# Kernel tuning notes

Measured on AMD Instinct MI355X. Metric: run time of the kernel, lower is better.

The kernel has to match this reference:

```python
import jax, jax.numpy as jnp
import numpy as np

B, N, D, E = 4, 1024, 1024, 8
TOP_N = 2
THRESHOLD = 0.2
EPS = 1e-9
CAP_FACTOR = 2.0
MIN_EXPERT_CAPACITY = 4
H = int(D * 4 * 2 / 3)  # GEGLU hidden = 2730


def setup_inputs() -> dict:
    key = jax.random.key(0)
    ks = jax.random.split(key, 8)
    u = lambda k, shape, fan: jax.random.uniform(k, shape, jnp.float32, -1.0, 1.0) * (fan ** -0.5)
    return {
        "x": jax.random.normal(ks[0], (B, N, D), jnp.float32),
        "route_probs": jax.random.uniform(ks[1], (TOP_N, B, N), jnp.float32),
        "gate_w": u(ks[2], (D, E), D),
        "w1": u(ks[3], (E, D, 2 * H), 2 * H),
        "b1": u(ks[4], (E, 2 * H), 2 * H),
        "mult_bias": jnp.ones((E, H), jnp.float32),
        "w2": u(ks[5], (E, H, D), D),
        "b2": u(ks[6], (E, D), D),
    }


def reference(x, route_probs, gate_w, w1, b1, mult_bias, w2, b2):
    b, n, d = x.shape
    e = gate_w.shape[1]
    cap = max(min(n, int(n * CAP_FACTOR / e)), MIN_EXPERT_CAPACITY)  # 256

    # ---- top-n gating ----
    logits = jnp.einsum('bnd,de->bne', x, gate_w)
    raw_gates = jax.nn.softmax(logits, axis=-1)
    gate_vals, gate_idx = jax.lax.top_k(raw_gates, TOP_N)          # [b,n,k]
    gate_vals = jnp.moveaxis(gate_vals, -1, 0)                      # [k,b,n]
    gate_idx = jnp.moveaxis(gate_idx, -1, 0)                        # [k,b,n]
    one_hot_idx = jax.nn.one_hot(gate_idx, e, dtype=x.dtype)        # [k,b,n,e]

    denom = jnp.clip(gate_vals.sum(axis=0, keepdims=True), EPS)
    gate_vals = gate_vals / denom

    # route to expert k>0 with prob min(1, gate/threshold); expert 0 always routed
    should_route = route_probs < (gate_vals / THRESHOLD)
    should_route = should_route.at[0].set(True)
    mask = one_hot_idx * should_route[..., None].astype(x.dtype)    # [k,b,n,e]

    # exclusive cumsum over sequence dim -> position within each expert
    mask_cumsum = jnp.cumsum(mask, axis=2) - mask                   # [k,b,n,e]

    positions, masks = [], []
    prev_count = jnp.zeros((b, 1, e), x.dtype)
    for k in range(TOP_N):  # small fixed loop over top-n
        pos_e = (mask_cumsum[k] + prev_count) * mask[k]             # [b,n,e]
        mk = mask[k] * (pos_e < float(cap)).astype(x.dtype)
        prev_count = prev_count + mk.sum(axis=1, keepdims=True)
        positions.append(pos_e.sum(axis=-1))                        # [b,n]
        masks.append(mk)
    positions = jnp.stack(positions)                                # [k,b,n]
    mask = jnp.stack(masks)                                         # [k,b,n,e]

    mask_flat = mask.sum(axis=-1)                                   # [k,b,n] in {0,1}
    gates = gate_vals * mask_flat
    pos_one_hot = jax.nn.one_hot(positions.astype(jnp.int32), cap, dtype=x.dtype)  # [k,b,n,c]

    # combine tensor [b,n,e,c]; dispatch is its boolean support
    combine = jnp.einsum('kbn,kbne,kbnc->bnec', gates * mask_flat, one_hot_idx, pos_one_hot)
    dispatch = (combine > 0).astype(x.dtype)

    # ---- dispatch tokens to experts ----
    xe = jnp.einsum('bnd,bnec->ebcd', x, dispatch)                  # [e,b,c,d]

    # ---- per-expert GEGLU FFN (grouped GEMM) ----
    h = jnp.einsum('ebcd,edf->ebcf', xe, w1) + b1[:, None, None, :]
    val, gate = jnp.split(h, 2, axis=-1)
    act = jax.nn.gelu(gate, approximate=False) * val * mult_bias[:, None, None, :]
    out_e = jnp.einsum('ebch,ehd->ebcd', act, w2) + b2[:, None, None, :]

    # ---- combine ----
    out = jnp.einsum('ebcd,bnec->bnd', out_e, combine)
    return out


if __name__ == '__main__':
    inp = setup_inputs()
    o = reference(**inp)
    print(o.shape, o.dtype)
```

## Files before the change

kernel.cpp:

```cpp
#include <hip/hip_runtime.h>
#include <hip/hip_bf16.h>
#include <math.h>

#define B_ 4
#define N_ 1024
#define D_ 1024
#define E_ 8
#define H_ 2730
#define H2_ 5460
#define CAP_ 256
#define NTOK 4096
#define NSLOT 8192
#define NKT1 16
#define NK1T 32
#define NKT2 43
#define NK2T 86
#define NFG 22

typedef __attribute__((ext_vector_type(8))) short short8;
typedef __attribute__((ext_vector_type(4))) float f32x4;

__device__ __forceinline__ unsigned short f2bf(float f) {
    __hip_bfloat16 h = __float2bfloat16(f);
    return *reinterpret_cast<unsigned short*>(&h);
}
__device__ __forceinline__ float bf2f(unsigned short u) {
    unsigned x = ((unsigned)u) << 16;
    union { unsigned u; float f; } c; c.u = x; return c.f;
}

#define GLL16(g, l)                                                          \
    __builtin_amdgcn_global_load_lds(                                        \
        (const __attribute__((address_space(1))) void*)(g),                  \
        (__attribute__((address_space(3))) void*)(l), 16, 0, 0)

#define VMCNT0() asm volatile("s_waitcnt vmcnt(0)" ::: "memory")
#define SBAR()   __builtin_amdgcn_s_barrier()
#define SCHEDB() __builtin_amdgcn_sched_barrier(0)
#define MFMA16(a, b, c) __builtin_amdgcn_mfma_f32_16x16x32_bf16((a), (b), (c), 0, 0, 0)


__global__ __launch_bounds__(256) void k_cvt1(const float* __restrict__ w1,
                                              unsigned short* __restrict__ w1p) {
    const int fg = blockIdx.x;
    const int kt = blockIdx.y;
    const int e  = blockIdx.z;
    const float* w1e = w1 + (size_t)e * D_ * H2_;
    unsigned short* dst = w1p + (((size_t)((e * NFG + fg) * NKT1 + kt)) << 14);
#pragma unroll
    for (int i = 0; i < 8; ++i) {
        const int o = i * 256 + threadIdx.x;
        const int l = o & 63, n16 = (o >> 6) & 15, k32 = o >> 10;
        const int f = fg * 128 + ((n16 & 7) << 4) + (l & 15);
        const int k = kt * 64 + (k32 << 5) + ((l >> 4) << 3);
        ushort4 r0 = {0, 0, 0, 0}, r1 = {0, 0, 0, 0};
        if (f < H_) {
            const float* s = w1e + (size_t)k * H2_ + (n16 >= 8 ? H_ : 0) + f;
            r0.x = f2bf(s[0]);
            r0.y = f2bf(s[(size_t)H2_]);
            r0.z = f2bf(s[(size_t)2 * H2_]);
            r0.w = f2bf(s[(size_t)3 * H2_]);
            r1.x = f2bf(s[(size_t)4 * H2_]);
            r1.y = f2bf(s[(size_t)5 * H2_]);
            r1.z = f2bf(s[(size_t)6 * H2_]);
            r1.w = f2bf(s[(size_t)7 * H2_]);
        }
        *reinterpret_cast<ushort4*>(dst + (size_t)o * 8) = r0;
        *reinterpret_cast<ushort4*>(dst + (size_t)o * 8 + 4) = r1;
    }
}

__global__ __launch_bounds__(256) void k_cvt2(const float* __restrict__ w2,
                                              unsigned short* __restrict__ w2p) {
    const int kt = blockIdx.x;
    const int nt = blockIdx.y;
    const int e  = blockIdx.z;
    const float* w2e = w2 + (size_t)e * H_ * D_;
    unsigned short* dst = w2p + (((size_t)((e * 8 + nt) * NKT2 + kt)) << 13);
#pragma unroll
    for (int i = 0; i < 4; ++i) {
        const int o = i * 256 + threadIdx.x;
        const int l = o & 63, n16 = (o >> 6) & 7, k32 = o >> 9;
        const int d = nt * 128 + (n16 << 4) + (l & 15);
        const int f = kt * 64 + (k32 << 5) + ((l >> 4) << 3);
        const float* s = w2e + (size_t)f * D_ + d;
        ushort4 r0, r1;
        r0.x = (f + 0 < H_) ? f2bf(s[0]) : 0;
        r0.y = (f + 1 < H_) ? f2bf(s[(size_t)D_]) : 0;
        r0.z = (f + 2 < H_) ? f2bf(s[(size_t)2 * D_]) : 0;
        r0.w = (f + 3 < H_) ? f2bf(s[(size_t)3 * D_]) : 0;
        r1.x = (f + 4 < H_) ? f2bf(s[(size_t)4 * D_]) : 0;
        r1.y = (f + 5 < H_) ? f2bf(s[(size_t)5 * D_]) : 0;
        r1.z = (f + 6 < H_) ? f2bf(s[(size_t)6 * D_]) : 0;
        r1.w = (f + 7 < H_) ? f2bf(s[(size_t)7 * D_]) : 0;
        *reinterpret_cast<ushort4*>(dst + (size_t)o * 8) = r0;
        *reinterpret_cast<ushort4*>(dst + (size_t)o * 8 + 4) = r1;
    }
}

__global__ __launch_bounds__(256) void k_gate(const float* __restrict__ x,
                                              const float* __restrict__ route,
                                              const float* __restrict__ gw,
                                              int* __restrict__ tokE,
                                              float* __restrict__ tokG,
                                              int* __restrict__ tokR) {
    const int wave = threadIdx.x >> 6, lane = threadIdx.x & 63;
    const int t = blockIdx.x * 4 + wave;
    float acc[E_];
#pragma unroll
    for (int e = 0; e < E_; ++e) acc[e] = 0.f;
    const float* xr = x + (size_t)t * D_;
    for (int d = lane; d < D_; d += 64) {
        float xv = xr[d];
        const float* g = gw + d * E_;
#pragma unroll
        for (int e = 0; e < E_; ++e) acc[e] = fmaf(xv, g[e], acc[e]);
    }
#pragma unroll
    for (int e = 0; e < E_; ++e) {
#pragma unroll
        for (int off = 32; off; off >>= 1) acc[e] += __shfl_xor(acc[e], off);
    }
    if (lane == 0) {
        float m = acc[0];
#pragma unroll
        for (int e = 1; e < E_; ++e) m = fmaxf(m, acc[e]);
        float p[E_]; float s = 0.f;
#pragma unroll
        for (int e = 0; e < E_; ++e) { p[e] = expf(acc[e] - m); s += p[e]; }
        int i0 = 0; float v0 = p[0];
#pragma unroll
        for (int e = 1; e < E_; ++e) if (p[e] > v0) { v0 = p[e]; i0 = e; }
        int i1 = (i0 == 0) ? 1 : 0; float v1 = p[i1];
#pragma unroll
        for (int e = 0; e < E_; ++e) if (e != i0 && p[e] > v1) { v1 = p[e]; i1 = e; }
        float p0 = v0 / s, p1 = v1 / s;
        float denom = fmaxf(p0 + p1, 1e-9f);
        float g0 = p0 / denom, g1 = p1 / denom;
        int r1 = route[NTOK + t] < (g1 / 0.2f);
        tokE[t] = i0; tokE[NTOK + t] = i1;
        tokG[t] = g0; tokG[NTOK + t] = g1;
        tokR[t] = r1;
    }
}

__global__ __launch_bounds__(256) void k_pos(const int* __restrict__ tokE,
                                             const float* __restrict__ tokG,
                                             const int* __restrict__ tokR,
                                             int* __restrict__ sot,
                                             int* __restrict__ tos) {
    const int e = blockIdx.x & 7, b = blockIdx.x >> 3;
    const int t = threadIdx.x;
    __shared__ int sc[256];
    const int base_bt = b * N_ + t * 4;
    int m0[4], m1[4];
    int c0 = 0, c1 = 0;
#pragma unroll
    for (int i = 0; i < 4; ++i) {
        int bt = base_bt + i;
        m0[i] = (tokE[bt] == e) ? 1 : 0;
        m1[i] = ((tokE[NTOK + bt] == e) && tokR[bt]) ? 1 : 0;
        c0 += m0[i]; c1 += m1[i];
    }
    int packed = c0 | (c1 << 16);
    sc[t] = packed;
    __syncthreads();
    for (int off = 1; off < 256; off <<= 1) {
        int v = (t >= off) ? sc[t - off] : 0;
        __syncthreads();
        sc[t] += v;
        __syncthreads();
    }
    int incl = sc[t];
    int total = sc[255];
    int excl = incl - packed;
    int base0 = excl & 0xffff;
    int base1 = excl >> 16;
    int kept0 = min(total & 0xffff, CAP_);
#pragma unroll
    for (int i = 0; i < 4; ++i) {
        int bt = base_bt + i;
        if (m0[i]) {
            int pos = base0++;
            if (pos < CAP_ && tokG[bt] > 0.f) {
                int s = ((e * B_ + b) << 8) + pos;
                sot[bt] = s;
                tos[s] = bt;
            }
        }
        if (m1[i]) {
            int pos = (base1++) + kept0;
            if (pos < CAP_ && tokG[NTOK + bt] > 0.f) {
                int s = ((e * B_ + b) << 8) + pos;
                sot[NTOK + bt] = s;
                tos[s] = bt;
            }
        }
    }
}

__global__ __launch_bounds__(256) void k_disp(const float* __restrict__ x,
                                              const int* __restrict__ tos,
                                              unsigned short* __restrict__ xeP) {
    const int t = threadIdx.x;
    const int s = blockIdx.x * 2 + (t >> 7);
    const int q = t & 127;
    const int bt = tos[s];
    const int kt = q >> 3, k32 = (q >> 2) & 1, kq = q & 3;
    const int lane = (kq << 4) | (s & 15);
    const int m16 = (s >> 4) & 15;
    const int sgrp = s >> 8;
    unsigned short* dst = xeP + (((size_t)(sgrp * NKT1 + kt)) << 14) + (k32 << 13) + (m16 << 9) + lane * 8;
    ushort4 r0 = {0, 0, 0, 0}, r1 = {0, 0, 0, 0};
    if (bt >= 0) {
        const float4 v0 = *reinterpret_cast<const float4*>(x + ((size_t)bt << 10) + q * 8);
        const float4 v1 = *reinterpret_cast<const float4*>(x + ((size_t)bt << 10) + q * 8 + 4);
        r0.x = f2bf(v0.x); r0.y = f2bf(v0.y); r0.z = f2bf(v0.z); r0.w = f2bf(v0.w);
        r1.x = f2bf(v1.x); r1.y = f2bf(v1.y); r1.z = f2bf(v1.z); r1.w = f2bf(v1.w);
    }
    *reinterpret_cast<ushort4*>(dst) = r0;
    *reinterpret_cast<ushort4*>(dst + 4) = r1;
}

#define LDF(BUF, idx) (*reinterpret_cast<const short8*>(&BUF[(idx) * 512 + lane8]))

#define F1TILE(ARD, BRD, AWR, BWR, KTN, PF)                                   \
    do {                                                                      \
        VMCNT0(); SBAR(); SCHEDB();                                           \
        if (PF) {                                                             \
            const unsigned short* as = abase + (size_t)(KTN) * 8192;          \
            const unsigned short* bs = bbase + (size_t)(KTN) * 8192;          \
            GLL16(as + t8, (char*)&AWR[t8_]);                                 \
            GLL16(as + 2048 + t8, (char*)&AWR[2048 + t8_]);                   \
            GLL16(bs + voff + t8, (char*)&BWR[t8_]);                          \
            GLL16(bs + goff + t8, (char*)&BWR[2048 + t8_]);                   \
        }                                                                     \
        SCHEDB();                                                             \
        short8 a0, a1, a2, a3, v0, v1, g0, g1;                                \
        a0 = LDF(ARD, am0 + 0); a1 = LDF(ARD, am0 + 1);                       \
        a2 = LDF(ARD, am0 + 2); a3 = LDF(ARD, am0 + 3);                       \
        v0 = LDF(BRD, bn0 + 0); v1 = LDF(BRD, bn0 + 1);                       \
        g0 = LDF(BRD, 4 + bn0 + 0); g1 = LDF(BRD, 4 + bn0 + 1);               \
        __builtin_amdgcn_s_setprio(1);                                        \
        acc[0][0]=MFMA16(a0,v0,acc[0][0]); acc[0][1]=MFMA16(a0,v1,acc[0][1]); \
        acc[0][2]=MFMA16(a0,g0,acc[0][2]); acc[0][3]=MFMA16(a0,g1,acc[0][3]); \
        acc[1][0]=MFMA16(a1,v0,acc[1][0]); acc[1][1]=MFMA16(a1,v1,acc[1][1]); \
        acc[1][2]=MFMA16(a1,g0,acc[1][2]); acc[1][3]=MFMA16(a1,g1,acc[1][3]); \
        acc[2][0]=MFMA16(a2,v0,acc[2][0]); acc[2][1]=MFMA16(a2,v1,acc[2][1]); \
        acc[2][2]=MFMA16(a2,g0,acc[2][2]); acc[2][3]=MFMA16(a2,g1,acc[2][3]); \
        acc[3][0]=MFMA16(a3,v0,acc[3][0]); acc[3][1]=MFMA16(a3,v1,acc[3][1]); \
        acc[3][2]=MFMA16(a3,g0,acc[3][2]); acc[3][3]=MFMA16(a3,g1,acc[3][3]); \
        __builtin_amdgcn_s_setprio(0);                                        \
    } while (0)

__global__ __launch_bounds__(256) void k_ffn1(const unsigned short* __restrict__ xeP,
                                              const unsigned short* __restrict__ w1p,
                                              const float* __restrict__ b1,
                                              const float* __restrict__ mbias,
                                              unsigned short* __restrict__ actP) {
    const int wg = blockIdx.x;
    const int e = wg & 7;
    const int rem = wg >> 3;
    const int fc = rem >> 3;
    const int rt = rem & 7;
    const int sgrp = e * 4 + (rt >> 1);
    const int half = rt & 1;
    const int fg = fc >> 1, hf = fc & 1;

    __shared__ unsigned short Ab0[4096];
    __shared__ unsigned short Bb0[4096];
    __shared__ unsigned short Ab1[4096];
    __shared__ unsigned short Bb1[4096];

    const int tid = threadIdx.x, lane = tid & 63, w = tid >> 6;
    const int wm = w >> 1, wn = w & 1;
    const int lane8 = lane * 8;
    const int t8 = tid * 8;
    const int t8_ = t8;
    const int am0 = wm * 4, bn0 = wn * 2;
    const int voff = hf * 2048;
    const int goff = 4096 + hf * 2048;

    const unsigned short* abase = xeP + ((size_t)(sgrp * NKT1) << 14) + half * 4096;
    const unsigned short* bbase = w1p + ((size_t)((e * NFG + fg) * NKT1) << 14);

    f32x4 acc[4][4];
#pragma unroll
    for (int i = 0; i < 4; ++i)
#pragma unroll
        for (int j = 0; j < 4; ++j) acc[i][j] = (f32x4)(0.f);

    GLL16(abase + t8, (char*)&Ab0[t8_]);
    GLL16(abase + 2048 + t8, (char*)&Ab0[2048 + t8_]);
    GLL16(bbase + voff + t8, (char*)&Bb0[t8_]);
    GLL16(bbase + goff + t8, (char*)&Bb0[2048 + t8_]);

    for (int kt = 0; kt < NK1T; kt += 2) {
        F1TILE(Ab0, Bb0, Ab1, Bb1, kt + 1, 1);
        F1TILE(Ab1, Bb1, Ab0, Bb0, kt + 2, (kt + 2) < NK1T);
    }

    const float* b1e = b1 + (size_t)e * H2_;
    const float* mbe = mbias + (size_t)e * H_;
    const int colL = lane & 15, rq4 = (lane >> 4) * 4;
#pragma unroll
    for (int mi = 0; mi < 4; ++mi) {
        const int rowbase = rt * 128 + wm * 64 + mi * 16;
        const int sg2 = e * 4 + (rowbase >> 8);
        const int m16w = (rowbase >> 4) & 15;
#pragma unroll
        for (int v = 0; v < 2; ++v) {
            const int f = fc * 64 + wn * 32 + v * 16 + colL;
            if (f >= NKT2 * 64) continue;
            const bool real = f < H_;
            const float bv = real ? b1e[f] : 0.f;
            const float bg = real ? b1e[H_ + f] : 0.f;
            const float mv = real ? mbe[f] : 0.f;
            const int ktf = f >> 6, k32f = (f >> 5) & 1;
            const int lhi = ((f >> 3) & 3) << 4;
            const int bb = f & 7;
            const size_t cbase = ((size_t)(sg2 * NKT2 + ktf) << 14) + (k32f << 13) + (m16w << 9);
#pragma unroll
            for (int j = 0; j < 4; ++j) {
                float a = 0.f;
                if (real) {
                    const float val = acc[mi][v][j] + bv;
                    const float gt  = acc[mi][2 + v][j] + bg;
                    a = 0.5f * gt * (1.f + erff(gt * 0.70710678118654752f)) * val * mv;
                }
                actP[cbase + (size_t)((lhi | (rq4 + j)) * 8 + bb)] = f2bf(a);
            }
        }
    }
}

#define F2TILE(ARD, BRD, AWR, BWR, KTN, PF)                                   \
    do {                                                                      \
        VMCNT0(); SBAR(); SCHEDB();                                           \
        if (PF) {                                                             \
            const unsigned short* as = abase + (size_t)(KTN) * 8192;          \
            const unsigned short* bs = bbase + (size_t)(KTN) * 4096;          \
            GLL16(as + t8, (char*)&AWR[t8]);                                  \
            GLL16(as + 2048 + t8, (char*)&AWR[2048 + t8]);                    \
            GLL16(bs + t8, (char*)&BWR[t8]);                                  \
            GLL16(bs + 2048 + t8, (char*)&BWR[2048 + t8]);                    \
        }                                                                     \
        SCHEDB();                                                             \
        short8 a0, a1, a2, a3, b0, b1, b2, b3;                                \
        a0 = LDF(ARD, am0 + 0); a1 = LDF(ARD, am0 + 1);                       \
        a2 = LDF(ARD, am0 + 2); a3 = LDF(ARD, am0 + 3);                       \
        b0 = LDF(BRD, bn4 + 0); b1 = LDF(BRD, bn4 + 1);                       \
        b2 = LDF(BRD, bn4 + 2); b3 = LDF(BRD, bn4 + 3);                       \
        __builtin_amdgcn_s_setprio(1);                                        \
        acc[0][0]=MFMA16(a0,b0,acc[0][0]); acc[0][1]=MFMA16(a0,b1,acc[0][1]); \
        acc[0][2]=MFMA16(a0,b2,acc[0][2]); acc[0][3]=MFMA16(a0,b3,acc[0][3]); \
        acc[1][0]=MFMA16(a1,b0,acc[1][0]); acc[1][1]=MFMA16(a1,b1,acc[1][1]); \
        acc[1][2]=MFMA16(a1,b2,acc[1][2]); acc[1][3]=MFMA16(a1,b3,acc[1][3]); \
        acc[2][0]=MFMA16(a2,b0,acc[2][0]); acc[2][1]=MFMA16(a2,b1,acc[2][1]); \
        acc[2][2]=MFMA16(a2,b2,acc[2][2]); acc[2][3]=MFMA16(a2,b3,acc[2][3]); \
        acc[3][0]=MFMA16(a3,b0,acc[3][0]); acc[3][1]=MFMA16(a3,b1,acc[3][1]); \
        acc[3][2]=MFMA16(a3,b2,acc[3][2]); acc[3][3]=MFMA16(a3,b3,acc[3][3]); \
        __builtin_amdgcn_s_setprio(0);                                        \
    } while (0)

__global__ __launch_bounds__(256) void k_ffn2(const unsigned short* __restrict__ actP,
                                              const unsigned short* __restrict__ w2p,
                                              const float* __restrict__ b2,
                                              unsigned short* __restrict__ oute) {
    const int wg = blockIdx.x;
    const int e = wg & 7;
    const int rem = wg >> 3;
    const int nt = rem >> 3;
    const int mt = rem & 7;
    const int sgrp = e * 4 + (mt >> 1);
    const int half = mt & 1;

    __shared__ unsigned short Ab0[4096];
    __shared__ unsigned short Bb0[4096];
    __shared__ unsigned short Ab1[4096];
    __shared__ unsigned short Bb1[4096];

    const int tid = threadIdx.x, lane = tid & 63, w = tid >> 6;
    const int wm = w >> 1, wn = w & 1;
    const int lane8 = lane * 8;
    const int t8 = tid * 8;
    const int am0 = wm * 4, bn4 = wn * 4;

    const unsigned short* abase = actP + ((size_t)(sgrp * NKT2) << 14) + half * 4096;
    const unsigned short* bbase = w2p + ((size_t)((e * 8 + nt) * NKT2) << 13);

    f32x4 acc[4][4];
#pragma unroll
    for (int i = 0; i < 4; ++i)
#pragma unroll
        for (int j = 0; j < 4; ++j) acc[i][j] = (f32x4)(0.f);

    GLL16(abase + t8, (char*)&Ab0[t8]);
    GLL16(abase + 2048 + t8, (char*)&Ab0[2048 + t8]);
    GLL16(bbase + t8, (char*)&Bb0[t8]);
    GLL16(bbase + 2048 + t8, (char*)&Bb0[2048 + t8]);

    for (int kt = 0; kt < NK2T; kt += 2) {
        F2TILE(Ab0, Bb0, Ab1, Bb1, kt + 1, 1);
        F2TILE(Ab1, Bb1, Ab0, Bb0, kt + 2, (kt + 2) < NK2T);
    }

    const float* b2e = b2 + (size_t)e * D_;
    const int colL = lane & 15, rq4 = (lane >> 4) * 4;
#pragma unroll
    for (int mi = 0; mi < 4; ++mi) {
#pragma unroll
        for (int nf = 0; nf < 4; ++nf) {
            const int d = nt * 128 + wn * 64 + nf * 16 + colL;
            const float bb2 = b2e[d];
#pragma unroll
            for (int j = 0; j < 4; ++j) {
                const int R = mt * 128 + wm * 64 + mi * 16 + rq4 + j;
                oute[((size_t)(e * 1024 + R) << 10) + d] = f2bf(acc[mi][nf][j] + bb2);
            }
        }
    }
}

__global__ __launch_bounds__(256) void k_comb(const unsigned short* __restrict__ oute,
                                              const int* __restrict__ sot,
                                              const float* __restrict__ tokG,
                                              float* __restrict__ out) {
    const int bt = blockIdx.x;
    const int t = threadIdx.x;
    const int s0 = sot[bt], s1 = sot[NTOK + bt];
    const float g0 = tokG[bt], g1 = tokG[NTOK + bt];
    float r0 = 0.f, r1 = 0.f, r2 = 0.f, r3 = 0.f;
    if (s0 >= 0) {
        const ushort4 v = *reinterpret_cast<const ushort4*>(oute + ((size_t)s0 << 10) + t * 4);
        r0 += g0 * bf2f(v.x); r1 += g0 * bf2f(v.y); r2 += g0 * bf2f(v.z); r3 += g0 * bf2f(v.w);
    }
    if (s1 >= 0) {
        const ushort4 v = *reinterpret_cast<const ushort4*>(oute + ((size_t)s1 << 10) + t * 4);
        r0 += g1 * bf2f(v.x); r1 += g1 * bf2f(v.y); r2 += g1 * bf2f(v.z); r3 += g1 * bf2f(v.w);
    }
    float4 o; o.x = r0; o.y = r1; o.z = r2; o.w = r3;
    *reinterpret_cast<float4*>(out + ((size_t)bt << 10) + t * 4) = o;
}

extern "C" void kernel_launch(void* const* d_in, const int* in_sizes, int n_in,
                              void* d_out, int out_size, void* d_ws, size_t ws_size,
                              hipStream_t stream) {
    const float* x     = (const float*)d_in[0];
    const float* route = (const float*)d_in[1];
    const float* gw    = (const float*)d_in[2];
    const float* w1    = (const float*)d_in[3];
    const float* b1    = (const float*)d_in[4];
    const float* mb    = (const float*)d_in[5];
    const float* w2    = (const float*)d_in[6];
    const float* b2    = (const float*)d_in[7];
    float* out = (float*)d_out;

    char* ws = (char*)d_ws;
    int*   tokE = (int*)(ws + 0);
    float* tokG = (float*)(ws + 32768);
    int*   tokR = (int*)(ws + 65536);
    int*   sot  = (int*)(ws + 81920);
    int*   tos  = (int*)(ws + 114688);
    unsigned short* xeP  = (unsigned short*)(ws + 147456);
    unsigned short* actP = (unsigned short*)(ws + 16924672);
    unsigned short* w1p  = (unsigned short*)(ws + 62013440);
    unsigned short* w2p  = (unsigned short*)(ws + 62013440);
    unsigned short* oute = (unsigned short*)(ws + 107102208);

    hipMemsetAsync(sot, 0xFF, 65536, stream);

    k_cvt1<<<dim3(NFG, NKT1, 8), 256, 0, stream>>>(w1, w1p);
    k_gate<<<NTOK / 4, 256, 0, stream>>>(x, route, gw, tokE, tokG, tokR);
    k_pos<<<E_ * B_, 256, 0, stream>>>(tokE, tokG, tokR, sot, tos);
    k_disp<<<NSLOT / 2, 256, 0, stream>>>(x, tos, xeP);
    k_ffn1<<<2752, 256, 0, stream>>>(xeP, w1p, b1, mb, actP);
    k_cvt2<<<dim3(NKT2, 8, 8), 256, 0, stream>>>(w2, w2p);
    k_ffn2<<<512, 256, 0, stream>>>(actP, w2p, b2, oute);
    k_comb<<<NTOK, 256, 0, stream>>>(oute, sot, tokG, out);
}
```

Measured before the change: 334.5 us.

## Use single-wave workgroups with barrier-free double-buffered GEMM pipelines in FFN kernels

Both FFN GEMM kernels now launch 64-thread single-wavefront workgroups, each owning a 64x64 output tile, instead of 256-thread workgroups with four waves sharing a 128x128 tile. Because each wave owns its own LDS buffers, the s_barrier is dropped. Synchronisation now uses vmcnt/lgkmcnt waits, with two k-tiles prefetched ahead and each buffer reloaded right after its fragments are read into registers. This targets barrier stalls and gives more workgroups to fill the GPU, but each wave now loads its own A and B tiles, so data reuse across waves is lost and global/L2 traffic goes up.

```diff
diff --git a/kernel.cpp b/kernel.cpp
--- a/kernel.cpp
+++ b/kernel.cpp
@@ -35,7 +35,8 @@
         (__attribute__((address_space(3))) void*)(l), 16, 0, 0)
 
 #define VMCNT0() asm volatile("s_waitcnt vmcnt(0)" ::: "memory")
-#define SBAR()   __builtin_amdgcn_s_barrier()
+#define VMW8()   asm volatile("s_waitcnt vmcnt(8)" ::: "memory")
+#define LGKM0()  asm volatile("s_waitcnt lgkmcnt(0)" ::: "memory")
 #define SCHEDB() __builtin_amdgcn_sched_barrier(0)
 #define MFMA16(a, b, c) __builtin_amdgcn_mfma_f32_16x16x32_bf16((a), (b), (c), 0, 0, 0)
 
@@ -222,25 +223,35 @@
     *reinterpret_cast<ushort4*>(dst + 4) = r1;
 }
 
-#define LDF(BUF, idx) (*reinterpret_cast<const short8*>(&BUF[(idx) * 512 + lane8]))
-
-#define F1TILE(ARD, BRD, AWR, BWR, KTN, PF)                                   \
+#define AOFF(t) (((size_t)((t) >> 1) << 14) + (size_t)(((t) & 1) * 8192))
+#define BOFF2(t) (((size_t)((t) >> 1) << 13) + (size_t)(((t) & 1) * 4096))
+
+#define F1T(ABUF, BBUF, KTN, LAST, PF)                                        \
     do {                                                                      \
-        VMCNT0(); SBAR(); SCHEDB();                                           \
-        if (PF) {                                                             \
-            const unsigned short* as = abase + (size_t)(KTN) * 8192;          \
-            const unsigned short* bs = bbase + (size_t)(KTN) * 8192;          \
-            GLL16(as + t8, (char*)&AWR[t8_]);                                 \
-            GLL16(as + 2048 + t8, (char*)&AWR[2048 + t8_]);                   \
-            GLL16(bs + voff + t8, (char*)&BWR[t8_]);                          \
-            GLL16(bs + goff + t8, (char*)&BWR[2048 + t8_]);                   \
-        }                                                                     \
+        if (LAST) { VMCNT0(); } else { VMW8(); }                              \
         SCHEDB();                                                             \
         short8 a0, a1, a2, a3, v0, v1, g0, g1;                                \
-        a0 = LDF(ARD, am0 + 0); a1 = LDF(ARD, am0 + 1);                       \
-        a2 = LDF(ARD, am0 + 2); a3 = LDF(ARD, am0 + 3);                       \
-        v0 = LDF(BRD, bn0 + 0); v1 = LDF(BRD, bn0 + 1);                       \
-        g0 = LDF(BRD, 4 + bn0 + 0); g1 = LDF(BRD, 4 + bn0 + 1);               \
+        a0 = *(const short8*)&ABUF[lane8];                                    \
+        a1 = *(const short8*)&ABUF[512 + lane8];                              \
+        a2 = *(const short8*)&ABUF[1024 + lane8];                             \
+        a3 = *(const short8*)&ABUF[1536 + lane8];                             \
+        v0 = *(const short8*)&BBUF[lane8];                                    \
+        v1 = *(const short8*)&BBUF[512 + lane8];                              \
+        g0 = *(const short8*)&BBUF[1024 + lane8];                             \
+        g1 = *(const short8*)&BBUF[1536 + lane8];                             \
+        LGKM0(); SCHEDB();                                                    \
+        if (PF) {                                                             \
+            const unsigned short* as = abase + AOFF(KTN);                     \
+            const unsigned short* bs = bbase + AOFF(KTN);                     \
+            GLL16(as + lane8, (char*)&ABUF[0]);                               \
+            GLL16(as + 512 + lane8, (char*)&ABUF[512]);                       \
+            GLL16(as + 1024 + lane8, (char*)&ABUF[1024]);                     \
+            GLL16(as + 1536 + lane8, (char*)&ABUF[1536]);                     \
+            GLL16(bs + lane8, (char*)&BBUF[0]);                               \
+            GLL16(bs + 512 + lane8, (char*)&BBUF[512]);                       \
+            GLL16(bs + 4096 + lane8, (char*)&BBUF[1024]);                     \
+            GLL16(bs + 4608 + lane8, (char*)&BBUF[1536]);                     \
+        }                                                                     \
         __builtin_amdgcn_s_setprio(1);                                        \
         acc[0][0]=MFMA16(a0,v0,acc[0][0]); acc[0][1]=MFMA16(a0,v1,acc[0][1]); \
         acc[0][2]=MFMA16(a0,g0,acc[0][2]); acc[0][3]=MFMA16(a0,g1,acc[0][3]); \
@@ -253,36 +264,31 @@
         __builtin_amdgcn_s_setprio(0);                                        \
     } while (0)
 
-__global__ __launch_bounds__(256) void k_ffn1(const unsigned short* __restrict__ xeP,
-                                              const unsigned short* __restrict__ w1p,
-                                              const float* __restrict__ b1,
-                                              const float* __restrict__ mbias,
-                                              unsigned short* __restrict__ actP) {
+__global__ __launch_bounds__(64) void k_ffn1(const unsigned short* __restrict__ xeP,
+                                             const unsigned short* __restrict__ w1p,
+                                             const float* __restrict__ b1,
+                                             const float* __restrict__ mbias,
+                                             unsigned short* __restrict__ actP) {
     const int wg = blockIdx.x;
     const int e = wg & 7;
     const int rem = wg >> 3;
-    const int fc = rem >> 3;
-    const int rt = rem & 7;
-    const int sgrp = e * 4 + (rt >> 1);
-    const int half = rt & 1;
-    const int fg = fc >> 1, hf = fc & 1;
-
-    __shared__ unsigned short Ab0[4096];
-    __shared__ unsigned short Bb0[4096];
-    __shared__ unsigned short Ab1[4096];
-    __shared__ unsigned short Bb1[4096];
-
-    const int tid = threadIdx.x, lane = tid & 63, w = tid >> 6;
-    const int wm = w >> 1, wn = w & 1;
+    const int fh = rem >> 4;
+    const int rb = rem & 15;
+    const int sgrp = e * 4 + (rb >> 2);
+    const int m16b = (rb & 3) * 4;
+    const int fg = fh >> 2;
+    const int n16v = (fh & 3) * 2;
+
+    __shared__ unsigned short A0[2048];
+    __shared__ unsigned short B0[2048];
+    __shared__ unsigned short A1[2048];
+    __shared__ unsigned short B1[2048];
+
+    const int lane = threadIdx.x;
     const int lane8 = lane * 8;
-    const int t8 = tid * 8;
-    const int t8_ = t8;
-    const int am0 = wm * 4, bn0 = wn * 2;
-    const int voff = hf * 2048;
-    const int goff = 4096 + hf * 2048;
-
-    const unsigned short* abase = xeP + ((size_t)(sgrp * NKT1) << 14) + half * 4096;
-    const unsigned short* bbase = w1p + ((size_t)((e * NFG + fg) * NKT1) << 14);
+
+    const unsigned short* abase = xeP + ((size_t)(sgrp * NKT1) << 14) + m16b * 512;
+    const unsigned short* bbase = w1p + ((size_t)((e * NFG + fg) * NKT1) << 14) + n16v * 512;
 
     f32x4 acc[4][4];
 #pragma unroll
@@ -290,14 +296,30 @@
 #pragma unroll
         for (int j = 0; j < 4; ++j) acc[i][j] = (f32x4)(0.f);
 
-    GLL16(abase + t8, (char*)&Ab0[t8_]);
-    GLL16(abase + 2048 + t8, (char*)&Ab0[2048 + t8_]);
-    GLL16(bbase + voff + t8, (char*)&Bb0[t8_]);
-    GLL16(bbase + goff + t8, (char*)&Bb0[2048 + t8_]);
-
-    for (int kt = 0; kt < NK1T; kt += 2) {
-        F1TILE(Ab0, Bb0, Ab1, Bb1, kt + 1, 1);
-        F1TILE(Ab1, Bb1, Ab0, Bb0, kt + 2, (kt + 2) < NK1T);
+    {
+        GLL16(abase + lane8, (char*)&A0[0]);
+        GLL16(abase + 512 + lane8, (char*)&A0[512]);
+        GLL16(abase + 1024 + lane8, (char*)&A0[1024]);
+        GLL16(abase + 1536 + lane8, (char*)&A0[1536]);
+        GLL16(bbase + lane8, (char*)&B0[0]);
+        GLL16(bbase + 512 + lane8, (char*)&B0[512]);
+        GLL16(bbase + 4096 + lane8, (char*)&B0[1024]);
+        GLL16(bbase + 4608 + lane8, (char*)&B0[1536]);
+        const unsigned short* as = abase + 8192;
+        const unsigned short* bs = bbase + 8192;
+        GLL16(as + lane8, (char*)&A1[0]);
+        GLL16(as + 512 + lane8, (char*)&A1[512]);
+        GLL16(as + 1024 + lane8, (char*)&A1[1024]);
+        GLL16(as + 1536 + lane8, (char*)&A1[1536]);
+        GLL16(bs + lane8, (char*)&B1[0]);
+        GLL16(bs + 512 + lane8, (char*)&B1[512]);
+        GLL16(bs + 4096 + lane8, (char*)&B1[1024]);
+        GLL16(bs + 4608 + lane8, (char*)&B1[1536]);
+    }
+
+    for (int t = 0; t < NK1T; t += 2) {
+        F1T(A0, B0, t + 2, 0, (t + 2) < NK1T);
+        F1T(A1, B1, t + 3, (t + 1) == NK1T - 1, (t + 3) < NK1T);
     }
 
     const float* b1e = b1 + (size_t)e * H2_;
@@ -305,13 +327,12 @@
     const int colL = lane & 15, rq4 = (lane >> 4) * 4;
 #pragma unroll
     for (int mi = 0; mi < 4; ++mi) {
-        const int rowbase = rt * 128 + wm * 64 + mi * 16;
+        const int rowbase = rb * 64 + mi * 16;
         const int sg2 = e * 4 + (rowbase >> 8);
         const int m16w = (rowbase >> 4) & 15;
 #pragma unroll
         for (int v = 0; v < 2; ++v) {
-            const int f = fc * 64 + wn * 32 + v * 16 + colL;
-            if (f >= NKT2 * 64) continue;
+            const int f = fh * 32 + v * 16 + colL;
             const bool real = f < H_;
             const float bv = real ? b1e[f] : 0.f;
             const float bg = real ? b1e[H_ + f] : 0.f;
@@ -334,23 +355,32 @@
     }
 }
 
-#define F2TILE(ARD, BRD, AWR, BWR, KTN, PF)                                   \
+#define F2T(ABUF, BBUF, KTN, LAST, PF)                                        \
     do {                                                                      \
-        VMCNT0(); SBAR(); SCHEDB();                                           \
-        if (PF) {                                                             \
-            const unsigned short* as = abase + (size_t)(KTN) * 8192;          \
-            const unsigned short* bs = bbase + (size_t)(KTN) * 4096;          \
-            GLL16(as + t8, (char*)&AWR[t8]);                                  \
-            GLL16(as + 2048 + t8, (char*)&AWR[2048 + t8]);                    \
-            GLL16(bs + t8, (char*)&BWR[t8]);                                  \
-            GLL16(bs + 2048 + t8, (char*)&BWR[2048 + t8]);                    \
-        }                                                                     \
+        if (LAST) { VMCNT0(); } else { VMW8(); }                              \
         SCHEDB();                                                             \
         short8 a0, a1, a2, a3, b0, b1, b2, b3;                                \
-        a0 = LDF(ARD, am0 + 0); a1 = LDF(ARD, am0 + 1);                       \
-        a2 = LDF(ARD, am0 + 2); a3 = LDF(ARD, am0 + 3);                       \
-        b0 = LDF(BRD, bn4 + 0); b1 = LDF(BRD, bn4 + 1);                       \
-        b2 = LDF(BRD, bn4 + 2); b3 = LDF(BRD, bn4 + 3);                       \
+        a0 = *(const short8*)&ABUF[lane8];                                    \
+        a1 = *(const short8*)&ABUF[512 + lane8];                              \
+        a2 = *(const short8*)&ABUF[1024 + lane8];                             \
+        a3 = *(const short8*)&ABUF[1536 + lane8];                             \
+        b0 = *(const short8*)&BBUF[lane8];                                    \
+        b1 = *(const short8*)&BBUF[512 + lane8];                              \
+        b2 = *(const short8*)&BBUF[1024 + lane8];                             \
+        b3 = *(const short8*)&BBUF[1536 + lane8];                             \
+        LGKM0(); SCHEDB();                                                    \
+        if (PF) {                                                             \
+            const unsigned short* as = abase + AOFF(KTN);                     \
+            const unsigned short* bs = bbase + BOFF2(KTN);                    \
+            GLL16(as + lane8, (char*)&ABUF[0]);                               \
+            GLL16(as + 512 + lane8, (char*)&ABUF[512]);                       \
+            GLL16(as + 1024 + lane8, (char*)&ABUF[1024]);                     \
+            GLL16(as + 1536 + lane8, (char*)&ABUF[1536]);                     \
+            GLL16(bs + lane8, (char*)&BBUF[0]);                               \
+            GLL16(bs + 512 + lane8, (char*)&BBUF[512]);                       \
+            GLL16(bs + 1024 + lane8, (char*)&BBUF[1024]);                     \
+            GLL16(bs + 1536 + lane8, (char*)&BBUF[1536]);                     \
+        }                                                                     \
         __builtin_amdgcn_s_setprio(1);                                        \
         acc[0][0]=MFMA16(a0,b0,acc[0][0]); acc[0][1]=MFMA16(a0,b1,acc[0][1]); \
         acc[0][2]=MFMA16(a0,b2,acc[0][2]); acc[0][3]=MFMA16(a0,b3,acc[0][3]); \
@@ -363,31 +393,29 @@
         __builtin_amdgcn_s_setprio(0);                                        \
     } while (0)
 
-__global__ __launch_bounds__(256) void k_ffn2(const unsigned short* __restrict__ actP,
-                                              const unsigned short* __restrict__ w2p,
-                                              const float* __restrict__ b2,
-                                              unsigned short* __restrict__ oute) {
+__global__ __launch_bounds__(64) void k_ffn2(const unsigned short* __restrict__ actP,
+                                             const unsigned short* __restrict__ w2p,
+                                             const float* __restrict__ b2,
+                                             unsigned short* __restrict__ oute) {
     const int wg = blockIdx.x;
     const int e = wg & 7;
     const int rem = wg >> 3;
-    const int nt = rem >> 3;
-    const int mt = rem & 7;
-    const int sgrp = e * 4 + (mt >> 1);
-    const int half = mt & 1;
-
-    __shared__ unsigned short Ab0[4096];
-    __shared__ unsigned short Bb0[4096];
-    __shared__ unsigned short Ab1[4096];
-    __shared__ unsigned short Bb1[4096];
-
-    const int tid = threadIdx.x, lane = tid & 63, w = tid >> 6;
-    const int wm = w >> 1, wn = w & 1;
+    const int db = rem >> 4;
+    const int rb = rem & 15;
+    const int sgrp = e * 4 + (rb >> 2);
+    const int m16b = (rb & 3) * 4;
+    const int n16b = (db & 1) * 4;
+
+    __shared__ unsigned short A0[2048];
+    __shared__ unsigned short B0[2048];
+    __shared__ unsigned short A1[2048];
+    __shared__ unsigned short B1[2048];
+
+    const int lane = threadIdx.x;
     const int lane8 = lane * 8;
-    const int t8 = tid * 8;
-    const int am0 = wm * 4, bn4 = wn * 4;
-
-    const unsigned short* abase = actP + ((size_t)(sgrp * NKT2) << 14) + half * 4096;
-    const unsigned short* bbase = w2p + ((size_t)((e * 8 + nt) * NKT2) << 13);
+
+    const unsigned short* abase = actP + ((size_t)(sgrp * NKT2) << 14) + m16b * 512;
+    const unsigned short* bbase = w2p + ((size_t)((e * 8 + (db >> 1)) * NKT2) << 13) + n16b * 512;
 
     f32x4 acc[4][4];
 #pragma unroll
@@ -395,14 +423,30 @@
 #pragma unroll
         for (int j = 0; j < 4; ++j) acc[i][j] = (f32x4)(0.f);
 
-    GLL16(abase + t8, (char*)&Ab0[t8]);
-    GLL16(abase + 2048 + t8, (char*)&Ab0[2048 + t8]);
-    GLL16(bbase + t8, (char*)&Bb0[t8]);
-    GLL16(bbase + 2048 + t8, (char*)&Bb0[2048 + t8]);
-
-    for (int kt = 0; kt < NK2T; kt += 2) {
-        F2TILE(Ab0, Bb0, Ab1, Bb1, kt + 1, 1);
-        F2TILE(Ab1, Bb1, Ab0, Bb0, kt + 2, (kt + 2) < NK2T);
+    {
+        GLL16(abase + lane8, (char*)&A0[0]);
+        GLL16(abase + 512 + lane8, (char*)&A0[512]);
+        GLL16(abase + 1024 + lane8, (char*)&A0[1024]);
+        GLL16(abase + 1536 + lane8, (char*)&A0[1536]);
+        GLL16(bbase + lane8, (char*)&B0[0]);
+        GLL16(bbase + 512 + lane8, (char*)&B0[512]);
+        GLL16(bbase + 1024 + lane8, (char*)&B0[1024]);
+        GLL16(bbase + 1536 + lane8, (char*)&B0[1536]);
+        const unsigned short* as = abase + 8192;
+        const unsigned short* bs = bbase + 4096;
+        GLL16(as + lane8, (char*)&A1[0]);
+        GLL16(as + 512 + lane8, (char*)&A1[512]);
+        GLL16(as + 1024 + lane8, (char*)&A1[1024]);
+        GLL16(as + 1536 + lane8, (char*)&A1[1536]);
+        GLL16(bs + lane8, (char*)&B1[0]);
+        GLL16(bs + 512 + lane8, (char*)&B1[512]);
+        GLL16(bs + 1024 + lane8, (char*)&B1[1024]);
+        GLL16(bs + 1536 + lane8, (char*)&B1[1536]);
+    }
+
+    for (int t = 0; t < NK2T; t += 2) {
+        F2T(A0, B0, t + 2, 0, (t + 2) < NK2T);
+        F2T(A1, B1, t + 3, (t + 1) == NK2T - 1, (t + 3) < NK2T);
     }
 
     const float* b2e = b2 + (size_t)e * D_;
@@ -411,11 +455,11 @@
     for (int mi = 0; mi < 4; ++mi) {
 #pragma unroll
         for (int nf = 0; nf < 4; ++nf) {
-            const int d = nt * 128 + wn * 64 + nf * 16 + colL;
+            const int d = db * 64 + nf * 16 + colL;
             const float bb2 = b2e[d];
 #pragma unroll
             for (int j = 0; j < 4; ++j) {
-                const int R = mt * 128 + wm * 64 + mi * 16 + rq4 + j;
+                const int R = rb * 64 + mi * 16 + rq4 + j;
                 oute[((size_t)(e * 1024 + R) << 10) + d] = f2bf(acc[mi][nf][j] + bb2);
             }
         }
@@ -474,8 +518,8 @@
     k_gate<<<NTOK / 4, 256, 0, stream>>>(x, route, gw, tokE, tokG, tokR);
     k_pos<<<E_ * B_, 256, 0, stream>>>(tokE, tokG, tokR, sot, tos);
     k_disp<<<NSLOT / 2, 256, 0, stream>>>(x, tos, xeP);
-    k_ffn1<<<2752, 256, 0, stream>>>(xeP, w1p, b1, mb, actP);
+    k_ffn1<<<11008, 64, 0, stream>>>(xeP, w1p, b1, mb, actP);
     k_cvt2<<<dim3(NKT2, 8, 8), 256, 0, stream>>>(w2, w2p);
-    k_ffn2<<<512, 256, 0, stream>>>(actP, w2p, b2, oute);
+    k_ffn2<<<2048, 64, 0, stream>>>(actP, w2p, b2, oute);
     k_comb<<<NTOK, 256, 0, stream>>>(oute, sot, tokG, out);
 }
```

Measured after the change: 349.1 us. 4.4% more time.
